# Optimization experiments

Hardware: AMD Instinct MI355X
Metric: run time of the kernel (lower is better)

Reference implementation:

```python
import jax, jax.numpy as jnp
import numpy as np

B, T, C, NH = 8, 512, 512, 8
HD = C // NH

def _layernorm(x, g, b, eps=1e-5):
    mu = jnp.mean(x, axis=-1, keepdims=True)
    var = jnp.var(x, axis=-1, keepdims=True)
    return (x - mu) * jax.lax.rsqrt(var + eps) * g + b

def setup_inputs() -> dict:
    key = jax.random.key(0)
    ks = jax.random.split(key, 5)
    return {
        "x": jax.random.normal(ks[0], (B, T, C), jnp.float32),
        "w_attn": jax.random.normal(ks[1], (3 * C, C), jnp.float32) * (1.0 / np.sqrt(C)),
        "b_attn": jnp.zeros((3 * C,), jnp.float32),
        "w_proj": jax.random.normal(ks[2], (C, C), jnp.float32) * (1.0 / np.sqrt(C)),
        "b_proj": jnp.zeros((C,), jnp.float32),
        "q_gamma": jnp.ones((C,), jnp.float32),
        "q_beta": jnp.zeros((C,), jnp.float32),
        "k_gamma": jnp.ones((C,), jnp.float32),
        "k_beta": jnp.zeros((C,), jnp.float32),
        "rel_emb": jax.random.normal(ks[3], (T, C), jnp.float32) * 0.02,
    }

def reference(x, w_attn, b_attn, w_proj, b_proj, q_gamma, q_beta, k_gamma, k_beta, rel_emb):
    b, t, c = x.shape
    # QKV projection (torch Linear: x @ W.T + b)
    qkv = x @ w_attn.T + b_attn                       # [B,T,3C]
    q, k, v = jnp.split(qkv, 3, axis=-1)
    # per-stream LayerNorm over full embedding dim (q_ln/k_ln = LayerNorm(n_embd))
    q = _layernorm(q, q_gamma, q_beta)
    k = _layernorm(k, k_gamma, k_beta)
    # split heads -> [B,NH,T,HD]
    q = q.reshape(b, t, NH, HD).transpose(0, 2, 1, 3)
    k = k.reshape(b, t, NH, HD).transpose(0, 2, 1, 3)
    v = v.reshape(b, t, NH, HD).transpose(0, 2, 1, 3)
    # relative-position bias: gather rel_emb[|i-j|] -> [T,T,NH,HD]
    idx = jnp.abs(jnp.arange(t)[None, :] - jnp.arange(t)[:, None])  # [T,T] int
    rel = rel_emb[idx].reshape(t, t, NH, HD)
    rel_bias = jnp.einsum("bhqd,qkhd->bhqk", q, rel)  # [B,NH,T,T]
    scale = 1.0 / np.sqrt(HD)
    scores = (jnp.einsum("bhqd,bhkd->bhqk", q, k) + rel_bias) * scale
    causal = jnp.tril(jnp.ones((t, t), bool))
    scores = jnp.where(causal[None, None], scores, jnp.finfo(scores.dtype).min)
    att = jax.nn.softmax(scores, axis=-1)
    y = jnp.einsum("bhqk,bhkd->bhqd", att, v)         # [B,NH,T,HD]
    y = y.transpose(0, 2, 1, 3).reshape(b, t, c)
    return y @ w_proj.T + b_proj
```

## Files before the change

### kernel.cpp

```cpp
#include <hip/hip_runtime.h>
#include <hip/hip_bf16.h>
#include <cstddef>

#define BB 8
#define TT 512
#define CC 512
#define NHH 8
#define HDD 64

typedef __attribute__((ext_vector_type(8))) short short8;
typedef __attribute__((ext_vector_type(4))) float f32x4;

__device__ __forceinline__ unsigned short f2bf(float f) {
    unsigned u = __float_as_uint(f);
    u += 0x7FFFu + ((u >> 16) & 1u);
    return (unsigned short)(u >> 16);
}
__device__ __forceinline__ float bf2f(unsigned short h) {
    return __uint_as_float(((unsigned)h) << 16);
}

__global__ __launch_bounds__(256) void cvt_k(
    const float* __restrict__ in, unsigned short* __restrict__ out)
{
    const int i = (blockIdx.x * 256 + threadIdx.x) * 4;
    const float4 v = *(const float4*)(in + i);
    unsigned short tmp[4] = {f2bf(v.x), f2bf(v.y), f2bf(v.z), f2bf(v.w)};
    *(uint2*)(out + i) = *(const uint2*)tmp;
}

__global__ __launch_bounds__(256, 2) void gemm_qkv_mfma(
    const unsigned short* __restrict__ Xb, const unsigned short* __restrict__ Wb,
    const float* __restrict__ bias, float* __restrict__ qkbuf,
    unsigned short* __restrict__ VT)
{
    __shared__ __align__(16) unsigned short lds[128 * 136];

    const int tid = threadIdx.x;
    const int w = tid >> 6, lane = tid & 63;
    const int c = lane & 15, quad = lane >> 4;
    const int wm = w >> 1, wn = w & 1;
    const int bm = blockIdx.y * 128, bn = blockIdx.x * 128;

    const unsigned short* pp[8];
#pragma unroll
    for (int l = 0; l < 8; ++l) {
        const int ci = w * 8 + l;
        if (ci < 16) {
            const int m16 = ci >> 1, kk = ci & 1;
            pp[l] = Xb + (size_t)(bm + m16 * 16 + c) * 512 + kk * 32 + quad * 8;
        } else {
            const int cb = ci - 16, n16 = cb >> 1, kk = cb & 1;
            pp[l] = Wb + (size_t)(bn + n16 * 16 + c) * 512 + kk * 32 + quad * 8;
        }
    }

    f32x4 acc[4][4];
#pragma unroll
    for (int i = 0; i < 4; ++i)
#pragma unroll
        for (int j = 0; j < 4; ++j) acc[i][j] = (f32x4){0.f, 0.f, 0.f, 0.f};

    short8 pre[8];
#pragma unroll
    for (int l = 0; l < 8; ++l) pre[l] = *(const short8*)pp[l];

    for (int k0 = 0; k0 < 512; k0 += 64) {
        __syncthreads();
#pragma unroll
        for (int l = 0; l < 8; ++l)
            *(short8*)&lds[(w * 8 + l) * 512 + lane * 8] = pre[l];
        __syncthreads();
        if (k0 + 64 < 512) {
#pragma unroll
            for (int l = 0; l < 8; ++l)
                pre[l] = *(const short8*)(pp[l] + k0 + 64);
        }
#pragma unroll
        for (int kk = 0; kk < 2; ++kk) {
            short8 af[4], bfr[4];
#pragma unroll
            for (int i = 0; i < 4; ++i)
                af[i] = *(const short8*)&lds[((wm * 4 + i) * 2 + kk) * 512 + lane * 8];
#pragma unroll
            for (int j = 0; j < 4; ++j)
                bfr[j] = *(const short8*)&lds[(16 + (wn * 4 + j) * 2 + kk) * 512 + lane * 8];
#pragma unroll
            for (int i = 0; i < 4; ++i)
#pragma unroll
                for (int j = 0; j < 4; ++j)
                    acc[i][j] = __builtin_amdgcn_mfma_f32_16x16x32_bf16(
                        af[i], bfr[j], acc[i][j], 0, 0, 0);
        }
    }

    float bj[4];
#pragma unroll
    for (int j = 0; j < 4; ++j) bj[j] = bias[bn + wn * 64 + j * 16 + c];

    if (bn < 1024) {
#pragma unroll
        for (int i = 0; i < 4; ++i)
#pragma unroll
            for (int j = 0; j < 4; ++j) {
                const int n = bn + wn * 64 + j * 16 + c;
#pragma unroll
                for (int r = 0; r < 4; ++r) {
                    const int m = bm + wm * 64 + i * 16 + quad * 4 + r;
                    qkbuf[(size_t)m * 1024 + n] = acc[i][j][r] + bj[j];
                }
            }
    } else {
        __syncthreads();
#pragma unroll
        for (int i = 0; i < 4; ++i)
#pragma unroll
            for (int j = 0; j < 4; ++j) {
                const int col = wn * 64 + j * 16 + c;
                const int row0 = wm * 64 + i * 16 + quad * 4;
                unsigned short t4[4];
#pragma unroll
                for (int r = 0; r < 4; ++r) t4[r] = f2bf(acc[i][j][r] + bj[j]);
                *(uint2*)&lds[col * 136 + row0] = *(const uint2*)t4;
            }
        __syncthreads();
        const int bi = bm >> 9, tb = bm & 511;
        const int hd0 = bn - 1024;
#pragma unroll
        for (int l = 0; l < 8; ++l) {
            const int idx = l * 256 + tid;
            const int col = idx >> 4, grp = idx & 15;
            const short8 v = *(const short8*)&lds[col * 136 + grp * 8];
            const int hd = hd0 + col, h = hd >> 6, d = hd & 63;
            *(short8*)(VT + ((size_t)(bi * NHH + h) * HDD + d) * TT + tb + grp * 8) = v;
        }
    }
}

__global__ __launch_bounds__(256) void ln_k(
    const float* __restrict__ qkbuf,
    const float* __restrict__ qg, const float* __restrict__ qb,
    const float* __restrict__ kg, const float* __restrict__ kb,
    unsigned short* __restrict__ Qh, unsigned short* __restrict__ Kh)
{
    const int row = blockIdx.x;
    const int bi = row >> 9, t = row & 511;
    const float* base = qkbuf + (size_t)row * 1024;
    const int tid = threadIdx.x;
    __shared__ float red[8];
    __shared__ float stat[2];

#pragma unroll
    for (int sstr = 0; sstr < 2; ++sstr) {
        const float* p = base + sstr * 512;
        const float* gam = sstr ? kg : qg;
        const float* bet = sstr ? kb : qb;
        unsigned short* outp = sstr ? Kh : Qh;
        const float v0 = p[tid];
        const float v1 = p[tid + 256];
        float sum = v0 + v1;
        float sq = v0 * v0 + v1 * v1;
#pragma unroll
        for (int off = 32; off > 0; off >>= 1) {
            sum += __shfl_down(sum, off);
            sq += __shfl_down(sq, off);
        }
        const int lane = tid & 63, wv = tid >> 6;
        if (lane == 0) { red[wv * 2] = sum; red[wv * 2 + 1] = sq; }
        __syncthreads();
        if (tid == 0) {
            const float ts = red[0] + red[2] + red[4] + red[6];
            const float tq = red[1] + red[3] + red[5] + red[7];
            const float mu = ts * (1.f / 512.f);
            const float var = tq * (1.f / 512.f) - mu * mu;
            stat[0] = mu;
            stat[1] = rsqrtf(var + 1e-5f);
        }
        __syncthreads();
        const float mu = stat[0], rsg = stat[1];
        const float o0 = (v0 - mu) * rsg * gam[tid] + bet[tid];
        const float o1 = (v1 - mu) * rsg * gam[tid + 256] + bet[tid + 256];
        const int c0 = tid, c1 = tid + 256;
        outp[((size_t)(bi * NHH + (c0 >> 6)) * TT + t) * HDD + (c0 & 63)] = f2bf(o0);
        outp[((size_t)(bi * NHH + (c1 >> 6)) * TT + t) * HDD + (c1 & 63)] = f2bf(o1);
        __syncthreads();
    }
}

__global__ __launch_bounds__(256, 2) void attn_k(
    const unsigned short* __restrict__ Qh, const unsigned short* __restrict__ Kh,
    const unsigned short* __restrict__ VT, const unsigned short* __restrict__ Relb,
    unsigned short* __restrict__ Yb)
{
    __shared__ __align__(16) unsigned short Qs[8 * 512];
    __shared__ __align__(16) unsigned short Ks[8 * 512];
    __shared__ __align__(16) unsigned short Vs[8 * 512];
    __shared__ __align__(16) unsigned short Rels[16 * 512];
    __shared__ __align__(16) unsigned short Ps[4][16 * 72];
    __shared__ __align__(16) unsigned short RDs[4][16 * 132];

    const int tid = threadIdx.x;
    const int w = tid >> 6;
    const int lane = tid & 63;
    const int c = lane & 15;
    const int quad = lane >> 4;
    const int qt = blockIdx.x, h = blockIdx.y, b = blockIdx.z;
    const int i0 = qt * 64;

    const unsigned short* Qbase = Qh + (size_t)(b * NHH + h) * TT * HDD;
    const unsigned short* Kbase = Kh + (size_t)(b * NHH + h) * TT * HDD;
    const unsigned short* Vbase = VT + (size_t)(b * NHH + h) * HDD * TT;
    const unsigned short* Rbase = Relb + h * HDD;

#pragma unroll
    for (int kk = 0; kk < 2; ++kk) {
        const unsigned short* gp =
            Qbase + (size_t)(i0 + w * 16 + c) * HDD + kk * 32 + quad * 8;
        *(short8*)&Qs[(w * 2 + kk) * 512 + lane * 8] = *(const short8*)gp;
    }

    f32x4 oacc[4];
    float m_i[4], l_i[4];
#pragma unroll
    for (int r = 0; r < 4; ++r) { m_i[r] = -1e30f; l_i[r] = 0.f; }
#pragma unroll
    for (int nd = 0; nd < 4; ++nd) oacc[nd] = (f32x4){0.f, 0.f, 0.f, 0.f};

    short8 aq0, aq1;

    for (int jt = 0; jt <= qt; ++jt) {
        const int j0 = jt * 64;
#pragma unroll
        for (int kk = 0; kk < 2; ++kk) {
            const unsigned short* gp =
                Kbase + (size_t)(j0 + w * 16 + c) * HDD + kk * 32 + quad * 8;
            *(short8*)&Ks[(w * 2 + kk) * 512 + lane * 8] = *(const short8*)gp;
        }
#pragma unroll
        for (int js = 0; js < 2; ++js) {
            const unsigned short* gp =
                Vbase + (size_t)(w * 16 + c) * TT + j0 + js * 32 + quad * 8;
            *(short8*)&Vs[(w * 2 + js) * 512 + lane * 8] = *(const short8*)gp;
        }
        const int mbase = i0 - j0 - 63;
#pragma unroll
        for (int sb = 0; sb < 2; ++sb) {
#pragma unroll
            for (int kk = 0; kk < 2; ++kk) {
                const int n16 = w * 2 + sb;
                int mrow = mbase + n16 * 16 + c;
                mrow = mrow < 0 ? 0 : (mrow > 511 ? 511 : mrow);
                const unsigned short* gp =
                    Rbase + (size_t)mrow * CC + kk * 32 + quad * 8;
                *(short8*)&Rels[(n16 * 2 + kk) * 512 + lane * 8] = *(const short8*)gp;
            }
        }
        __syncthreads();

        if (jt == 0) {
            aq0 = *(const short8*)&Qs[(w * 2 + 0) * 512 + lane * 8];
            aq1 = *(const short8*)&Qs[(w * 2 + 1) * 512 + lane * 8];
        }

        f32x4 sAcc[4];
#pragma unroll
        for (int ns = 0; ns < 4; ++ns) {
            const short8 bk0 = *(const short8*)&Ks[(ns * 2 + 0) * 512 + lane * 8];
            const short8 bk1 = *(const short8*)&Ks[(ns * 2 + 1) * 512 + lane * 8];
            f32x4 a2 = (f32x4){0.f, 0.f, 0.f, 0.f};
            a2 = __builtin_amdgcn_mfma_f32_16x16x32_bf16(aq0, bk0, a2, 0, 0, 0);
            a2 = __builtin_amdgcn_mfma_f32_16x16x32_bf16(aq1, bk1, a2, 0, 0, 0);
            sAcc[ns] = a2;
        }
#pragma unroll
        for (int nr = 0; nr < 8; ++nr) {
            const short8 br0 = *(const short8*)&Rels[(nr * 2 + 0) * 512 + lane * 8];
            const short8 br1 = *(const short8*)&Rels[(nr * 2 + 1) * 512 + lane * 8];
            f32x4 a2 = (f32x4){0.f, 0.f, 0.f, 0.f};
            a2 = __builtin_amdgcn_mfma_f32_16x16x32_bf16(aq0, br0, a2, 0, 0, 0);
            a2 = __builtin_amdgcn_mfma_f32_16x16x32_bf16(aq1, br1, a2, 0, 0, 0);
#pragma unroll
            for (int r = 0; r < 4; ++r)
                RDs[w][(quad * 4 + r) * 132 + nr * 16 + c] = f2bf(a2[r]);
        }

        float sc[4][4];
#pragma unroll
        for (int ns = 0; ns < 4; ++ns) {
#pragma unroll
            for (int r = 0; r < 4; ++r) {
                const int r16 = quad * 4 + r;
                const int jc = ns * 16 + c;
                const int dp = w * 16 + r16 - jc + 63;
                const float rdv = bf2f(RDs[w][r16 * 132 + dp]);
                const float v = (sAcc[ns][r] + rdv) * 0.125f;
                sc[ns][r] = (j0 + jc > i0 + w * 16 + r16) ? -1e30f : v;
            }
        }
        float alpha[4];
#pragma unroll
        for (int r = 0; r < 4; ++r) {
            float m = fmaxf(fmaxf(sc[0][r], sc[1][r]), fmaxf(sc[2][r], sc[3][r]));
#pragma unroll
            for (int off = 1; off < 16; off <<= 1) m = fmaxf(m, __shfl_xor(m, off));
            const float mn = fmaxf(m_i[r], m);
            alpha[r] = __expf(m_i[r] - mn);
            m_i[r] = mn;
        }
        float rs[4] = {0.f, 0.f, 0.f, 0.f};
#pragma unroll
        for (int ns = 0; ns < 4; ++ns) {
#pragma unroll
            for (int r = 0; r < 4; ++r) {
                const float p = __expf(sc[ns][r] - m_i[r]);
                rs[r] += p;
                Ps[w][(quad * 4 + r) * 72 + ns * 16 + c] = f2bf(p);
            }
        }
#pragma unroll
        for (int r = 0; r < 4; ++r) {
#pragma unroll
            for (int off = 1; off < 16; off <<= 1) rs[r] += __shfl_xor(rs[r], off);
            l_i[r] = l_i[r] * alpha[r] + rs[r];
        }
#pragma unroll
        for (int nd = 0; nd < 4; ++nd)
#pragma unroll
            for (int r = 0; r < 4; ++r) oacc[nd][r] *= alpha[r];

        const short8 ap0 = *(const short8*)&Ps[w][c * 72 + 0 * 32 + quad * 8];
        const short8 ap1 = *(const short8*)&Ps[w][c * 72 + 1 * 32 + quad * 8];
#pragma unroll
        for (int nd = 0; nd < 4; ++nd) {
            const short8 bv0 = *(const short8*)&Vs[(nd * 2 + 0) * 512 + lane * 8];
            const short8 bv1 = *(const short8*)&Vs[(nd * 2 + 1) * 512 + lane * 8];
            oacc[nd] = __builtin_amdgcn_mfma_f32_16x16x32_bf16(ap0, bv0, oacc[nd], 0, 0, 0);
            oacc[nd] = __builtin_amdgcn_mfma_f32_16x16x32_bf16(ap1, bv1, oacc[nd], 0, 0, 0);
        }
        __syncthreads();
    }

#pragma unroll
    for (int r = 0; r < 4; ++r) {
        const float inv = 1.f / l_i[r];
        const int trow = i0 + w * 16 + quad * 4 + r;
        unsigned short* yb = Yb + ((size_t)b * TT + trow) * CC + h * HDD;
#pragma unroll
        for (int nd = 0; nd < 4; ++nd)
            yb[nd * 16 + c] = f2bf(oacc[nd][r] * inv);
    }
}

__global__ __launch_bounds__(256, 2) void gemm_proj_mfma(
    const unsigned short* __restrict__ Yb, const unsigned short* __restrict__ Wp,
    const float* __restrict__ bias, float* __restrict__ out)
{
    __shared__ __align__(16) unsigned short lds[24 * 512];

    const int tid = threadIdx.x;
    const int w = tid >> 6, lane = tid & 63;
    const int c = lane & 15, quad = lane >> 4;
    const int wm = w >> 1, wn = w & 1;
    const int bm = blockIdx.y * 64, bn = blockIdx.x * 128;

    const unsigned short* pp[6];
#pragma unroll
    for (int l = 0; l < 6; ++l) {
        const int ci = w * 6 + l;
        if (ci < 8) {
            const int m16 = ci >> 1, kk = ci & 1;
            pp[l] = Yb + (size_t)(bm + m16 * 16 + c) * 512 + kk * 32 + quad * 8;
        } else {
            const int cb = ci - 8, n16 = cb >> 1, kk = cb & 1;
            pp[l] = Wp + (size_t)(bn + n16 * 16 + c) * 512 + kk * 32 + quad * 8;
        }
    }

    f32x4 acc[2][4];
#pragma unroll
    for (int i = 0; i < 2; ++i)
#pragma unroll
        for (int j = 0; j < 4; ++j) acc[i][j] = (f32x4){0.f, 0.f, 0.f, 0.f};

    short8 pre[6];
#pragma unroll
    for (int l = 0; l < 6; ++l) pre[l] = *(const short8*)pp[l];

    for (int k0 = 0; k0 < 512; k0 += 64) {
        __syncthreads();
#pragma unroll
        for (int l = 0; l < 6; ++l)
            *(short8*)&lds[(w * 6 + l) * 512 + lane * 8] = pre[l];
        __syncthreads();
        if (k0 + 64 < 512) {
#pragma unroll
            for (int l = 0; l < 6; ++l)
                pre[l] = *(const short8*)(pp[l] + k0 + 64);
        }
#pragma unroll
        for (int kk = 0; kk < 2; ++kk) {
            short8 af[2], bfr[4];
#pragma unroll
            for (int i = 0; i < 2; ++i)
                af[i] = *(const short8*)&lds[((wm * 2 + i) * 2 + kk) * 512 + lane * 8];
#pragma unroll
            for (int j = 0; j < 4; ++j)
                bfr[j] = *(const short8*)&lds[(8 + (wn * 4 + j) * 2 + kk) * 512 + lane * 8];
#pragma unroll
            for (int i = 0; i < 2; ++i)
#pragma unroll
                for (int j = 0; j < 4; ++j)
                    acc[i][j] = __builtin_amdgcn_mfma_f32_16x16x32_bf16(
                        af[i], bfr[j], acc[i][j], 0, 0, 0);
        }
    }

#pragma unroll
    for (int j = 0; j < 4; ++j) {
        const int n = bn + wn * 64 + j * 16 + c;
        const float bj = bias[n];
#pragma unroll
        for (int i = 0; i < 2; ++i)
#pragma unroll
            for (int r = 0; r < 4; ++r) {
                const int m = bm + wm * 32 + i * 16 + quad * 4 + r;
                out[(size_t)m * 512 + n] = acc[i][j][r] + bj;
            }
    }
}

extern "C" void kernel_launch(void* const* d_in, const int* in_sizes, int n_in,
                              void* d_out, int out_size, void* d_ws, size_t ws_size,
                              hipStream_t stream)
{
    const float* x      = (const float*)d_in[0];
    const float* w_attn = (const float*)d_in[1];
    const float* b_attn = (const float*)d_in[2];
    const float* w_proj = (const float*)d_in[3];
    const float* b_proj = (const float*)d_in[4];
    const float* q_g    = (const float*)d_in[5];
    const float* q_b    = (const float*)d_in[6];
    const float* k_g    = (const float*)d_in[7];
    const float* k_b    = (const float*)d_in[8];
    const float* rel    = (const float*)d_in[9];
    float* out = (float*)d_out;

    float* qkbuf = (float*)d_ws;
    unsigned short* Qh   = (unsigned short*)(qkbuf + (size_t)4096 * 1024);
    unsigned short* Kh   = Qh + (size_t)4096 * 512;
    unsigned short* VT   = Kh + (size_t)4096 * 512;
    unsigned short* Relb = VT + (size_t)4096 * 512;
    unsigned short* Xb   = Relb + (size_t)512 * 512;
    unsigned short* Wqb  = Xb + (size_t)4096 * 512;
    unsigned short* Wpb  = Wqb + (size_t)1536 * 512;
    unsigned short* Yb   = (unsigned short*)qkbuf;

    cvt_k<<<2048, 256, 0, stream>>>(x, Xb);
    cvt_k<<<768, 256, 0, stream>>>(w_attn, Wqb);
    cvt_k<<<256, 256, 0, stream>>>(w_proj, Wpb);
    cvt_k<<<256, 256, 0, stream>>>(rel, Relb);
    gemm_qkv_mfma<<<dim3(12, 32), 256, 0, stream>>>(Xb, Wqb, b_attn, qkbuf, VT);
    ln_k<<<4096, 256, 0, stream>>>(qkbuf, q_g, q_b, k_g, k_b, Qh, Kh);
    attn_k<<<dim3(8, 8, 8), 256, 0, stream>>>(Qh, Kh, VT, Relb, Yb);
    gemm_proj_mfma<<<dim3(4, 64), 256, 0, stream>>>(Yb, Wpb, b_proj, out);
}
```

Baseline: 156.7 us.

## Reuse relative-position scores across key tiles via ring buffer; fuse conversion kernels

The attention kernel now treats the relative-position dot products as a 128-wide ring buffer indexed modulo 128. After the first key tile it loads and computes only the 64 new diagonal offsets instead of all 128, reusing the overlapping half from the previous iteration. This halves the rel_emb loads and the rel MFMAs per iteration. The four fp32-to-bf16 conversion launches are also merged into one kernel that picks its input and output per block range. This relies on RDs persisting correctly across iterations; the modulo indexing must match the overlap exactly.

```diff
diff --git a/kernel.cpp b/kernel.cpp
--- a/kernel.cpp
+++ b/kernel.cpp
@@ -20,10 +20,21 @@
     return __uint_as_float(((unsigned)h) << 16);
 }
 
-__global__ __launch_bounds__(256) void cvt_k(
-    const float* __restrict__ in, unsigned short* __restrict__ out)
-{
-    const int i = (blockIdx.x * 256 + threadIdx.x) * 4;
+__global__ __launch_bounds__(256) void cvt_all_k(
+    const float* __restrict__ x, const float* __restrict__ wa,
+    const float* __restrict__ wp, const float* __restrict__ rel,
+    unsigned short* __restrict__ Xb, unsigned short* __restrict__ Wqb,
+    unsigned short* __restrict__ Wpb, unsigned short* __restrict__ Relb)
+{
+    const int bidx = blockIdx.x;
+    const float* in;
+    unsigned short* out;
+    int base;
+    if (bidx < 2048)      { in = x;   out = Xb;   base = bidx; }
+    else if (bidx < 2816) { in = wa;  out = Wqb;  base = bidx - 2048; }
+    else if (bidx < 3072) { in = wp;  out = Wpb;  base = bidx - 2816; }
+    else                  { in = rel; out = Relb; base = bidx - 3072; }
+    const int i = base * 1024 + threadIdx.x * 4;
     const float4 v = *(const float4*)(in + i);
     unsigned short tmp[4] = {f2bf(v.x), f2bf(v.y), f2bf(v.z), f2bf(v.w)};
     *(uint2*)(out + i) = *(const uint2*)tmp;
@@ -187,6 +198,19 @@
     }
 }
 
+#define RD_BODY(nr_)                                                            \
+    {                                                                           \
+        const short8 br0 = *(const short8*)&Rels[((nr_) * 2 + 0) * 512 + lane * 8]; \
+        const short8 br1 = *(const short8*)&Rels[((nr_) * 2 + 1) * 512 + lane * 8]; \
+        f32x4 a2 = (f32x4){0.f, 0.f, 0.f, 0.f};                                 \
+        a2 = __builtin_amdgcn_mfma_f32_16x16x32_bf16(aq0, br0, a2, 0, 0, 0);    \
+        a2 = __builtin_amdgcn_mfma_f32_16x16x32_bf16(aq1, br1, a2, 0, 0, 0);    \
+        const int colw = (mbase + (nr_) * 16 + c) & 127;                        \
+        _Pragma("unroll")                                                       \
+        for (int r = 0; r < 4; ++r)                                             \
+            RDs[w][(quad * 4 + r) * 132 + colw] = f2bf(a2[r]);                  \
+    }
+
 __global__ __launch_bounds__(256, 2) void attn_k(
     const unsigned short* __restrict__ Qh, const unsigned short* __restrict__ Kh,
     const unsigned short* __restrict__ VT, const unsigned short* __restrict__ Relb,
@@ -243,16 +267,25 @@
             *(short8*)&Vs[(w * 2 + js) * 512 + lane * 8] = *(const short8*)gp;
         }
         const int mbase = i0 - j0 - 63;
-#pragma unroll
-        for (int sb = 0; sb < 2; ++sb) {
+        if (jt == 0) {
+#pragma unroll
+            for (int sb = 0; sb < 2; ++sb) {
+#pragma unroll
+                for (int kk = 0; kk < 2; ++kk) {
+                    const int n16 = w * 2 + sb;
+                    int mrow = mbase + n16 * 16 + c;
+                    mrow = mrow < 0 ? 0 : (mrow > 511 ? 511 : mrow);
+                    *(short8*)&Rels[(n16 * 2 + kk) * 512 + lane * 8] =
+                        *(const short8*)(Rbase + (size_t)mrow * CC + kk * 32 + quad * 8);
+                }
+            }
+        } else {
 #pragma unroll
             for (int kk = 0; kk < 2; ++kk) {
-                const int n16 = w * 2 + sb;
-                int mrow = mbase + n16 * 16 + c;
+                int mrow = mbase + w * 16 + c;
                 mrow = mrow < 0 ? 0 : (mrow > 511 ? 511 : mrow);
-                const unsigned short* gp =
-                    Rbase + (size_t)mrow * CC + kk * 32 + quad * 8;
-                *(short8*)&Rels[(n16 * 2 + kk) * 512 + lane * 8] = *(const short8*)gp;
+                *(short8*)&Rels[(w * 2 + kk) * 512 + lane * 8] =
+                    *(const short8*)(Rbase + (size_t)mrow * CC + kk * 32 + quad * 8);
             }
         }
         __syncthreads();
@@ -272,18 +305,15 @@
             a2 = __builtin_amdgcn_mfma_f32_16x16x32_bf16(aq1, bk1, a2, 0, 0, 0);
             sAcc[ns] = a2;
         }
-#pragma unroll
-        for (int nr = 0; nr < 8; ++nr) {
-            const short8 br0 = *(const short8*)&Rels[(nr * 2 + 0) * 512 + lane * 8];
-            const short8 br1 = *(const short8*)&Rels[(nr * 2 + 1) * 512 + lane * 8];
-            f32x4 a2 = (f32x4){0.f, 0.f, 0.f, 0.f};
-            a2 = __builtin_amdgcn_mfma_f32_16x16x32_bf16(aq0, br0, a2, 0, 0, 0);
-            a2 = __builtin_amdgcn_mfma_f32_16x16x32_bf16(aq1, br1, a2, 0, 0, 0);
-#pragma unroll
-            for (int r = 0; r < 4; ++r)
-                RDs[w][(quad * 4 + r) * 132 + nr * 16 + c] = f2bf(a2[r]);
-        }
-
+        if (jt == 0) {
+#pragma unroll
+            for (int nr = 0; nr < 8; ++nr) RD_BODY(nr)
+        } else {
+#pragma unroll
+            for (int nr = 0; nr < 4; ++nr) RD_BODY(nr)
+        }
+
+        const int dbase = i0 - j0;
         float sc[4][4];
 #pragma unroll
         for (int ns = 0; ns < 4; ++ns) {
@@ -291,7 +321,7 @@
             for (int r = 0; r < 4; ++r) {
                 const int r16 = quad * 4 + r;
                 const int jc = ns * 16 + c;
-                const int dp = w * 16 + r16 - jc + 63;
+                const int dp = (dbase + w * 16 + r16 - jc) & 127;
                 const float rdv = bf2f(RDs[w][r16 * 132 + dp]);
                 const float v = (sAcc[ns][r] + rdv) * 0.125f;
                 sc[ns][r] = (j0 + jc > i0 + w * 16 + r16) ? -1e30f : v;
@@ -455,10 +485,7 @@
     unsigned short* Wpb  = Wqb + (size_t)1536 * 512;
     unsigned short* Yb   = (unsigned short*)qkbuf;
 
-    cvt_k<<<2048, 256, 0, stream>>>(x, Xb);
-    cvt_k<<<768, 256, 0, stream>>>(w_attn, Wqb);
-    cvt_k<<<256, 256, 0, stream>>>(w_proj, Wpb);
-    cvt_k<<<256, 256, 0, stream>>>(rel, Relb);
+    cvt_all_k<<<3328, 256, 0, stream>>>(x, w_attn, w_proj, rel, Xb, Wqb, Wpb, Relb);
     gemm_qkv_mfma<<<dim3(12, 32), 256, 0, stream>>>(Xb, Wqb, b_attn, qkbuf, VT);
     ln_k<<<4096, 256, 0, stream>>>(qkbuf, q_g, q_b, k_g, k_b, Qh, Kh);
     attn_k<<<dim3(8, 8, 8), 256, 0, stream>>>(Qh, Kh, VT, Relb, Yb);
```

After: 149.6 us. -4.5%, faster.
